# Performance work log

Measured on AMD Instinct MI355X. Metric: run time of the kernel, lower is better.

The kernel has to match this reference:

```python
import jax, jax.numpy as jnp
import numpy as np

D = 1024

def setup_inputs() -> dict:
    key = jax.random.key(0)
    ks = jax.random.split(key, 9)
    s = 1.0 / np.sqrt(D)
    x = jax.random.normal(ks[0], (8, 4096, D), dtype=jnp.float32)
    Wq = jax.random.uniform(ks[1], (D, D), jnp.float32, -s, s)
    bq = jax.random.uniform(ks[2], (D,), jnp.float32, -s, s)
    Wk = jax.random.uniform(ks[3], (D, D), jnp.float32, -s, s)
    bk = jax.random.uniform(ks[4], (D,), jnp.float32, -s, s)
    Wv = jax.random.uniform(ks[5], (D, D), jnp.float32, -s, s)
    bv = jax.random.uniform(ks[6], (D,), jnp.float32, -s, s)
    Wo = jax.random.uniform(ks[7], (D, D), jnp.float32, -s, s)
    bo = jax.random.uniform(ks[8], (D,), jnp.float32, -s, s)
    return {"x": x, "Wq": Wq, "bq": bq, "Wk": Wk, "bk": bk,
            "Wv": Wv, "bv": bv, "Wo": Wo, "bo": bo}

def reference(x, Wq, bq, Wk, bk, Wv, bv, Wo, bo):
    # Linear projections (torch Linear: x @ W.T + b)
    Q = x @ Wq.T + bq
    K = x @ Wk.T + bk
    V = x @ Wv.T + bv
    # elu+1 feature map (positive features)
    Q = jax.nn.elu(Q) + 1.0
    K = jax.nn.elu(K) + 1.0
    # KV outer-product accumulation over sequence: [b, d, e]
    KV = jnp.einsum('bnd,bne->bde', K, V)
    # normalizer Z: [b, n]
    Z = jnp.einsum('bnd,bd->bn', Q, K.sum(axis=1) + 1e-6)
    context = jnp.einsum('bnd,bde->bne', Q, KV) / Z[..., None]
    return context @ Wo.T + bo
```

## Files before the change

kernel.cpp:

```cpp
#include <hip/hip_runtime.h>
#include <stdint.h>

typedef unsigned short u16;
typedef __attribute__((ext_vector_type(8))) short short8;
typedef __attribute__((ext_vector_type(4))) float f32x4;

#define SEQ    4096
#define NB     8
#define DMODEL 1024
#define MTOT   (NB*SEQ)

static __device__ __forceinline__ float bf2f(u16 u){
  union { float f; uint32_t i; } v; v.i = ((uint32_t)u) << 16; return v.f;
}
static __device__ __forceinline__ u16 f2bf(float f){
  union { float f; uint32_t i; } v; v.f = f;
  uint32_t i = v.i + 0x7FFFu + ((v.i >> 16) & 1u);
  return (u16)(i >> 16);
}

static __device__ __forceinline__ void stage16(const void* g, void* l){
  __builtin_amdgcn_global_load_lds(
      (const __attribute__((address_space(1))) void*)g,
      (__attribute__((address_space(3))) void*)l,
      16, 0, 0);
}

__global__ void cvt_f32_bf16(const float* __restrict__ s, u16* __restrict__ d, int n){
  int i = (blockIdx.x * 256 + threadIdx.x) * 8;
  if (i >= n) return;
  float4 a = *(const float4*)(s + i);
  float4 b = *(const float4*)(s + i + 4);
  union { u16 h[8]; short8 v; } o;
  o.h[0]=f2bf(a.x); o.h[1]=f2bf(a.y); o.h[2]=f2bf(a.z); o.h[3]=f2bf(a.w);
  o.h[4]=f2bf(b.x); o.h[5]=f2bf(b.y); o.h[6]=f2bf(b.z); o.h[7]=f2bf(b.w);
  *(short8*)(d + i) = o.v;
}

__global__ __launch_bounds__(256)
void cvt_tr(const float* __restrict__ in, u16* __restrict__ outN,
            u16* __restrict__ outT, int R, int C)
{
  __shared__ float t[64][65];
  const int tid = threadIdx.x;
  const int ntc = C >> 6;
  const int tr = blockIdx.x / ntc, tc = blockIdx.x % ntc;
  const int r0 = tr << 6, c0 = tc << 6;
  const int lrow = tid >> 4, lc4 = (tid & 15) << 2;
  #pragma unroll
  for (int p = 0; p < 4; p++){
    float4 v = *(const float4*)(in + (size_t)(r0 + p*16 + lrow) * C + c0 + lc4);
    t[p*16 + lrow][lc4+0] = v.x; t[p*16 + lrow][lc4+1] = v.y;
    t[p*16 + lrow][lc4+2] = v.z; t[p*16 + lrow][lc4+3] = v.w;
  }
  __syncthreads();
  const int wrow = tid >> 3, wc8 = (tid & 7) << 3;
  if (outN){
    #pragma unroll
    for (int p = 0; p < 2; p++){
      int r = p*32 + wrow;
      union { u16 h[8]; short8 v; } o;
      #pragma unroll
      for (int j = 0; j < 8; j++) o.h[j] = f2bf(t[r][wc8 + j]);
      *(short8*)(outN + (size_t)(r0 + r) * C + c0 + wc8) = o.v;
    }
  }
  #pragma unroll
  for (int p = 0; p < 2; p++){
    int c = p*32 + wrow;
    union { u16 h[8]; short8 v; } o;
    #pragma unroll
    for (int j = 0; j < 8; j++) o.h[j] = f2bf(t[wc8 + j][c]);
    *(short8*)(outT + (size_t)(c0 + c) * R + r0 + wc8) = o.v;
  }
}

__global__ void bo2_kernel(const float* __restrict__ Wo, const float* __restrict__ bv,
                           const float* __restrict__ bo, float* __restrict__ bo2){
  int o = blockIdx.x * 4 + (threadIdx.x >> 6);
  int lane = threadIdx.x & 63;
  const float* row = Wo + (size_t)o * DMODEL;
  float s = 0.f;
  #pragma unroll
  for (int j = 0; j < 4; j++){
    float4 w = *(const float4*)(row + j*256 + lane*4);
    float4 b = *(const float4*)(bv  + j*256 + lane*4);
    s += w.x*b.x + w.y*b.y + w.z*b.z + w.w*b.w;
  }
  for (int off = 32; off; off >>= 1) s += __shfl_xor(s, off);
  if (lane == 0) bo2[o] = bo[o] + s;
}

__global__ void ksum_kernel(const u16* __restrict__ Kt, float* __restrict__ Ksum){
  int wid  = blockIdx.x * 4 + (threadIdx.x >> 6);
  int lane = threadIdx.x & 63;
  int d = wid & 1023, b = wid >> 10;
  const u16* row = Kt + (size_t)d * MTOT + (size_t)b * SEQ;
  float s = 0.f;
  #pragma unroll
  for (int j = 0; j < 8; j++){
    short8 v = *(const short8*)(row + j * 512 + lane * 8);
    #pragma unroll
    for (int t = 0; t < 8; t++) s += bf2f((u16)v[t]);
  }
  for (int off = 32; off; off >>= 1) s += __shfl_xor(s, off);
  if (lane == 0) Ksum[wid] = s + 1e-6f;
}

__global__ void z_kernel(const u16* __restrict__ Qb, const float* __restrict__ Ksum,
                         float* __restrict__ Z){
  int n    = blockIdx.x * 4 + (threadIdx.x >> 6);
  int lane = threadIdx.x & 63;
  const u16*   qrow = Qb + (size_t)n * DMODEL;
  const float* ks   = Ksum + (size_t)(n >> 12) * DMODEL;
  float s = 0.f;
  #pragma unroll
  for (int j = 0; j < 2; j++){
    int base = j * 512 + lane * 8;
    short8 q  = *(const short8*)(qrow + base);
    float4 k0 = *(const float4*)(ks + base);
    float4 k1 = *(const float4*)(ks + base + 4);
    s += bf2f((u16)q[0])*k0.x + bf2f((u16)q[1])*k0.y + bf2f((u16)q[2])*k0.z + bf2f((u16)q[3])*k0.w
       + bf2f((u16)q[4])*k1.x + bf2f((u16)q[5])*k1.y + bf2f((u16)q[6])*k1.z + bf2f((u16)q[7])*k1.w;
  }
  for (int off = 32; off; off >>= 1) s += __shfl_xor(s, off);
  if (lane == 0) Z[n] = s;
}

__global__ __launch_bounds__(256)
void gemm_bt(const u16* __restrict__ A, int ldA,
             const u16* __restrict__ BT, int ldBT, int Kdim,
             u16* __restrict__ Obf, int ldO)
{
  __shared__ u16 Al[128 * 32];
  __shared__ u16 Bl[128 * 32];
  const int tid  = threadIdx.x;
  const int lane = tid & 63;
  const int w    = tid >> 6;
  const int tcol = blockIdx.x;
  const int trow = blockIdx.y;

  const u16* Ap = A  + (size_t)trow * 128 * ldA;
  const u16* Bp = BT + (size_t)tcol * 128 * ldBT;

  f32x4 acc[4][4] = {};
  const int srow = (lane >> 2);
  const int scol = (lane & 3) * 8;

  for (int k0 = 0; k0 < Kdim; k0 += 32){
    #pragma unroll
    for (int i = 0; i < 2; i++){
      int r = w * 32 + i * 16 + srow;
      stage16(Ap + (size_t)r * ldA  + k0 + scol, (char*)Al + w * 2048 + i * 1024);
      stage16(Bp + (size_t)r * ldBT + k0 + scol, (char*)Bl + w * 2048 + i * 1024);
    }
    __syncthreads();
    const int mr = (w >> 1) * 64, nc = (w & 1) * 64;
    const int lr = lane & 15, lk = (lane >> 4) * 8;
    short8 av[4], bv[4];
    #pragma unroll
    for (int mi = 0; mi < 4; mi++) av[mi] = *(const short8*)&Al[(mr + mi*16 + lr)*32 + lk];
    #pragma unroll
    for (int nj = 0; nj < 4; nj++) bv[nj] = *(const short8*)&Bl[(nc + nj*16 + lr)*32 + lk];
    #pragma unroll
    for (int mi = 0; mi < 4; mi++)
      #pragma unroll
      for (int nj = 0; nj < 4; nj++)
        acc[mi][nj] = __builtin_amdgcn_mfma_f32_16x16x32_bf16(av[mi], bv[nj], acc[mi][nj], 0, 0, 0);
    __syncthreads();
  }

  const int mr = (w >> 1) * 64, nc = (w & 1) * 64;
  const int lr = lane & 15, lq = lane >> 4;
  #pragma unroll
  for (int mi = 0; mi < 4; mi++)
    #pragma unroll
    for (int r = 0; r < 4; r++){
      const size_t grow = (size_t)trow * 128 + mr + mi * 16 + lq * 4 + r;
      #pragma unroll
      for (int nj = 0; nj < 4; nj++){
        const size_t gcol = (size_t)tcol * 128 + nc + nj * 16 + lr;
        Obf[grow * ldO + gcol] = f2bf(acc[mi][nj][r]);
      }
    }
}

static __device__ __forceinline__ void stage_chunk(
    const u16* __restrict__ g, int ld, int k0, u16* smem, int baseU16, int tid){
  #pragma unroll
  for (int c = 0; c < 2; c++){
    int lin = c * 512 + tid;
    int row = lin >> 3;
    int slotL = (lin & 7) ^ (row & 7);
    stage16(g + (size_t)row * ld + k0 + slotL * 8,
            (char*)smem + baseU16 * 2 + (c * 8 + (tid >> 6)) * 1024);
  }
}

template<int EPI>
__global__ __launch_bounds__(512, 2)
void gemm8(const u16* __restrict__ A, int ldA,
           const u16* __restrict__ BT, int ldBT, int NT,
           const float* __restrict__ bias, const float* __restrict__ Zv,
           u16* __restrict__ Obf, float* __restrict__ Of32, int ldO)
{
  __shared__ u16 smem[65536];
  const int tid  = threadIdx.x;
  const int lane = tid & 63;
  const int w    = tid >> 6;
  const int wm   = w >> 2, wn = w & 3;
  const int lr   = lane & 15, kq = lane >> 4;

  const int nwg  = gridDim.x;
  const int orig = blockIdx.x;
  const int work = (orig & 7) * (nwg >> 3) + (orig >> 3);
  int trow, tcol; size_t boff = 0;
  if (EPI == 1)      { trow = work & 3; tcol = work >> 2; }
  else               { tcol = work & 3; trow = work >> 2;
                       if (EPI == 2) boff = (size_t)(trow >> 4) * 1024; }
  const int tileM = trow * 256, tileN = tcol * 256;

  const u16* Ag = A + (size_t)tileM * ldA;
  const u16* Bg = BT + boff + (size_t)tileN * ldBT;

  f32x4 acc[8][4] = {};

#define STAGE(buf, k0) do { \
    stage_chunk(Ag,                    ldA,  (k0), smem, (buf) + 0,     tid); \
    stage_chunk(Ag + (size_t)128*ldA,  ldA,  (k0), smem, (buf) + 8192,  tid); \
    stage_chunk(Bg,                    ldBT, (k0), smem, (buf) + 16384, tid); \
    stage_chunk(Bg + (size_t)128*ldBT, ldBT, (k0), smem, (buf) + 24576, tid); \
  } while(0)

#define LDSA(MF, KC) (*(const short8*)(smem + cb + (wm*128 + (MF)*16 + lr)*64 + ((((KC)*4 + kq) ^ (lr & 7)) * 8)))
#define LDSB(NF, KC) (*(const short8*)(smem + cb + 16384 + (wn*64 + (NF)*16 + lr)*64 + ((((KC)*4 + kq) ^ (lr & 7)) * 8)))

#define QUAD(M0, N0, AV, BV) do { \
  __builtin_amdgcn_s_setprio(1); \
  _Pragma("unroll") for (int mi = 0; mi < 4; mi++) \
    _Pragma("unroll") for (int ni = 0; ni < 2; ni++) \
      _Pragma("unroll") for (int kc = 0; kc < 2; kc++) \
        acc[(M0)+mi][(N0)+ni] = __builtin_amdgcn_mfma_f32_16x16x32_bf16( \
            AV[mi][kc], BV[ni][kc], acc[(M0)+mi][(N0)+ni], 0, 0, 0); \
  __builtin_amdgcn_s_setprio(0); \
} while(0)

  STAGE(0, 0);
  STAGE(32768, 64);
  asm volatile("s_waitcnt vmcnt(8)" ::: "memory");
  __builtin_amdgcn_s_barrier();

  for (int t = 0; t < NT; t++){
    const int cb  = (t & 1) << 15;
    const int kNN = (t + 2 < NT ? t + 2 : NT - 1) * 64;
    short8 a0[4][2], a1[4][2], bl[2][2], bh[2][2];

    #pragma unroll
    for (int i = 0; i < 4; i++){ a0[i][0] = LDSA(i, 0);   a0[i][1] = LDSA(i, 1); }
    #pragma unroll
    for (int i = 0; i < 2; i++){ bl[i][0] = LDSB(i, 0);   bl[i][1] = LDSB(i, 1); }
    __builtin_amdgcn_s_barrier();
    asm volatile("s_waitcnt lgkmcnt(0)" ::: "memory");
    QUAD(0, 0, a0, bl);
    __builtin_amdgcn_s_barrier();

    #pragma unroll
    for (int i = 0; i < 2; i++){ bh[i][0] = LDSB(2+i, 0); bh[i][1] = LDSB(2+i, 1); }
    __builtin_amdgcn_s_barrier();
    asm volatile("s_waitcnt lgkmcnt(0)" ::: "memory");
    QUAD(0, 2, a0, bh);
    __builtin_amdgcn_s_barrier();

    #pragma unroll
    for (int i = 0; i < 4; i++){ a1[i][0] = LDSA(4+i, 0); a1[i][1] = LDSA(4+i, 1); }
    stage_chunk(Bg, ldBT, kNN, smem, cb + 16384, tid);
    __builtin_amdgcn_s_barrier();
    asm volatile("s_waitcnt lgkmcnt(0)" ::: "memory");
    QUAD(4, 2, a1, bh);
    __builtin_amdgcn_s_barrier();

    stage_chunk(Bg + (size_t)128*ldBT, ldBT, kNN, smem, cb + 24576, tid);
    stage_chunk(Ag,                    ldA,  kNN, smem, cb + 0,     tid);
    stage_chunk(Ag + (size_t)128*ldA,  ldA,  kNN, smem, cb + 8192,  tid);
    QUAD(4, 0, a1, bl);
    asm volatile("s_waitcnt vmcnt(8)" ::: "memory");
    __builtin_amdgcn_s_barrier();
  }

#undef STAGE
#undef LDSA
#undef LDSB
#undef QUAD

  #pragma unroll
  for (int mf = 0; mf < 8; mf++){
    #pragma unroll
    for (int r = 0; r < 4; r++){
      const int grow = tileM + wm*128 + mf*16 + kq*4 + r;
      float rowB = 0.f, zin = 0.f;
      if (EPI == 1) rowB = bias[grow];
      if (EPI == 2) zin = 1.f / Zv[grow];
      #pragma unroll
      for (int nf = 0; nf < 4; nf++){
        const int gcol = tileN + wn*64 + nf*16 + lr;
        float v = acc[mf][nf][r];
        if (EPI == 0) { v += bias[gcol]; v = (v > 0.f) ? v + 1.f : __expf(v); }
        if (EPI == 1) { v += rowB;       v = (v > 0.f) ? v + 1.f : __expf(v); }
        if constexpr (EPI == 2) Of32[(size_t)grow * ldO + gcol] = v * zin + bias[gcol];
        else                    Obf [(size_t)grow * ldO + gcol] = f2bf(v);
      }
    }
  }
}

template<int EPI>
__global__ __launch_bounds__(512, 2)
void gemm8h(const u16* __restrict__ A, int ldA,
            const u16* __restrict__ BT, int ldBT, int NT,
            u16* __restrict__ Obf, int ldO)
{
  __shared__ u16 smem[49152];
  const int tid  = threadIdx.x;
  const int lane = tid & 63;
  const int w    = tid >> 6;
  const int wm   = w >> 2, wn = w & 3;
  const int lr   = lane & 15, kq = lane >> 4;

  const int orig = blockIdx.x;
  const int work = (orig & 7) * 32 + (orig >> 3);
  int trow, tcol; size_t aoff = 0, boff = 0, ooff = 0;
  if (EPI == 3) { int zb = work >> 5, sub = work & 31;
                  trow = sub & 7; tcol = sub >> 3;
                  aoff = (size_t)zb * SEQ; boff = aoff; ooff = (size_t)zb << 20; }
  else          { trow = work & 7; tcol = work >> 3; }
  const int tileM = trow * 128, tileN = tcol * 256;

  const u16* Ag = A  + aoff + (size_t)tileM * ldA;
  const u16* Bg = BT + boff + (size_t)tileN * ldBT;

  f32x4 acc[4][4] = {};

#define STAGEH(buf, k0) do { \
    stage_chunk(Ag,                    ldA,  (k0), smem, (buf) + 0,     tid); \
    stage_chunk(Bg,                    ldBT, (k0), smem, (buf) + 8192,  tid); \
    stage_chunk(Bg + (size_t)128*ldBT, ldBT, (k0), smem, (buf) + 16384, tid); \
  } while(0)

#define LDSAH(MF, KC) (*(const short8*)(smem + cb + (wm*64 + (MF)*16 + lr)*64 + ((((KC)*4 + kq) ^ (lr & 7)) * 8)))
#define LDSBH(NF, KC) (*(const short8*)(smem + cb + 8192 + (wn*64 + (NF)*16 + lr)*64 + ((((KC)*4 + kq) ^ (lr & 7)) * 8)))

  STAGEH(0, 0);
  STAGEH(24576, 64);
  asm volatile("s_waitcnt vmcnt(6)" ::: "memory");
  __builtin_amdgcn_sched_barrier(0);
  __builtin_amdgcn_s_barrier();

  for (int t = 0; t < NT; t++){
    const int cb = (t & 1) * 24576;
    short8 af[4][2], bf[4][2];
    #pragma unroll
    for (int i = 0; i < 4; i++){ af[i][0] = LDSAH(i, 0); af[i][1] = LDSAH(i, 1); }
    #pragma unroll
    for (int i = 0; i < 4; i++){ bf[i][0] = LDSBH(i, 0); bf[i][1] = LDSBH(i, 1); }
    __builtin_amdgcn_s_setprio(1);
    #pragma unroll
    for (int mi = 0; mi < 4; mi++)
      #pragma unroll
      for (int nj = 0; nj < 4; nj++)
        #pragma unroll
        for (int kc = 0; kc < 2; kc++)
          acc[mi][nj] = __builtin_amdgcn_mfma_f32_16x16x32_bf16(
              af[mi][kc], bf[nj][kc], acc[mi][nj], 0, 0, 0);
    __builtin_amdgcn_s_setprio(0);
    __builtin_amdgcn_sched_barrier(0);
    __builtin_amdgcn_s_barrier();
    const int kNN = (t + 2 < NT ? t + 2 : NT - 1) * 64;
    STAGEH(cb, kNN);
    asm volatile("s_waitcnt vmcnt(6)" ::: "memory");
    __builtin_amdgcn_sched_barrier(0);
    __builtin_amdgcn_s_barrier();
  }
#undef STAGEH
#undef LDSAH
#undef LDSBH

  #pragma unroll
  for (int mf = 0; mf < 4; mf++){
    #pragma unroll
    for (int r = 0; r < 4; r++){
      const int grow = tileM + wm*64 + mf*16 + kq*4 + r;
      #pragma unroll
      for (int nf = 0; nf < 4; nf++){
        const int gcol = tileN + wn*64 + nf*16 + lr;
        Obf[ooff + (size_t)grow * ldO + gcol] = f2bf(acc[mf][nf][r]);
      }
    }
  }
}

extern "C" void kernel_launch(void* const* d_in, const int* in_sizes, int n_in,
                              void* d_out, int out_size, void* d_ws, size_t ws_size,
                              hipStream_t stream)
{
  const float* x  = (const float*)d_in[0];
  const float* Wq = (const float*)d_in[1];
  const float* bq = (const float*)d_in[2];
  const float* Wk = (const float*)d_in[3];
  const float* bk = (const float*)d_in[4];
  const float* Wv = (const float*)d_in[5];
  const float* bv = (const float*)d_in[6];
  const float* Wo = (const float*)d_in[7];
  const float* bo = (const float*)d_in[8];
  float* out = (float*)d_out;

  char* ws = (char*)d_ws;
  u16*   xb  = (u16*)(ws + 0);
  u16*   Tt  = (u16*)(ws + 0);
  u16*   Gt  = (u16*)(ws + 16777216);
  u16*   xT  = (u16*)(ws + 67108864);
  u16*   Qb  = (u16*)(ws + 134217728);
  u16*   Kt  = (u16*)(ws + 201326592);
  u16*   Wqb = (u16*)(ws + 268435456);
  u16*   Wkb = (u16*)(ws + 270532608);
  u16*   Wob = (u16*)(ws + 272629760);
  u16*   WvT = (u16*)(ws + 274726912);
  u16*   W2b = (u16*)(ws + 276824064);
  float* Ks  = (float*)(ws + 278921216);
  float* Zp  = (float*)(ws + 278953984);
  float* bo2 = (float*)(ws + 279085056);

  cvt_tr<<<8192, 256, 0, stream>>>(x, xb, xT, MTOT, DMODEL);
  cvt_f32_bf16<<<512, 256, 0, stream>>>(Wq, Wqb, DMODEL * DMODEL);
  cvt_f32_bf16<<<512, 256, 0, stream>>>(Wk, Wkb, DMODEL * DMODEL);
  cvt_f32_bf16<<<512, 256, 0, stream>>>(Wo, Wob, DMODEL * DMODEL);
  cvt_tr<<<256, 256, 0, stream>>>(Wv, (u16*)nullptr, WvT, DMODEL, DMODEL);
  bo2_kernel<<<256, 256, 0, stream>>>(Wo, bv, bo, bo2);
  gemm_bt<<<dim3(8, 8, 1), dim3(256), 0, stream>>>(Wob, 1024, WvT, 1024, 1024,
                                                   W2b, 1024);

  gemm8<0><<<512, 512, 0, stream>>>(xb, 1024, Wqb, 1024, 16, bq, nullptr,
                                    Qb, nullptr, 1024);
  gemm8<1><<<512, 512, 0, stream>>>(Wkb, 1024, xb, 1024, 16, bk, nullptr,
                                    Kt, nullptr, MTOT);
  ksum_kernel<<<2048, 256, 0, stream>>>(Kt, Ks);
  z_kernel<<<8192, 256, 0, stream>>>(Qb, Ks, Zp);
  gemm8h<3><<<256, 512, 0, stream>>>(Kt, MTOT, xT, MTOT, 64, Tt, 1024);
  gemm8h<4><<<256, 512, 0, stream>>>(W2b, 1024, Tt, 1024, 16, Gt, 8192);
  gemm8<2><<<512, 512, 0, stream>>>(Qb, 1024, Gt, 8192, 16, bo2, Zp,
                                    nullptr, out, 1024);
}
```

Measured before the change: 428.7 us.

## Fuse K-sum and Z normalizer reductions into projection GEMM epilogues

Removes the separate ksum and z kernels. The K-sum and Z dot products are now computed inside the K- and Q-projection GEMM epilogues using shuffle reductions and atomicAdd, after a memset of the accumulators. Each gemm8 block now computes two adjacent 256-column tiles in sequence, keeping the A rows in the pipeline, and the grid is halved to 256 blocks. The cost is atomic contention and order-dependent float sums, and the K GEMM must now run before the Q GEMM. Halving the grid may also leave CUs underused.

```diff
diff --git a/kernel.cpp b/kernel.cpp
--- a/kernel.cpp
+++ b/kernel.cpp
@@ -89,42 +89,6 @@
   }
   for (int off = 32; off; off >>= 1) s += __shfl_xor(s, off);
   if (lane == 0) bo2[o] = bo[o] + s;
-}
-
-__global__ void ksum_kernel(const u16* __restrict__ Kt, float* __restrict__ Ksum){
-  int wid  = blockIdx.x * 4 + (threadIdx.x >> 6);
-  int lane = threadIdx.x & 63;
-  int d = wid & 1023, b = wid >> 10;
-  const u16* row = Kt + (size_t)d * MTOT + (size_t)b * SEQ;
-  float s = 0.f;
-  #pragma unroll
-  for (int j = 0; j < 8; j++){
-    short8 v = *(const short8*)(row + j * 512 + lane * 8);
-    #pragma unroll
-    for (int t = 0; t < 8; t++) s += bf2f((u16)v[t]);
-  }
-  for (int off = 32; off; off >>= 1) s += __shfl_xor(s, off);
-  if (lane == 0) Ksum[wid] = s + 1e-6f;
-}
-
-__global__ void z_kernel(const u16* __restrict__ Qb, const float* __restrict__ Ksum,
-                         float* __restrict__ Z){
-  int n    = blockIdx.x * 4 + (threadIdx.x >> 6);
-  int lane = threadIdx.x & 63;
-  const u16*   qrow = Qb + (size_t)n * DMODEL;
-  const float* ks   = Ksum + (size_t)(n >> 12) * DMODEL;
-  float s = 0.f;
-  #pragma unroll
-  for (int j = 0; j < 2; j++){
-    int base = j * 512 + lane * 8;
-    short8 q  = *(const short8*)(qrow + base);
-    float4 k0 = *(const float4*)(ks + base);
-    float4 k1 = *(const float4*)(ks + base + 4);
-    s += bf2f((u16)q[0])*k0.x + bf2f((u16)q[1])*k0.y + bf2f((u16)q[2])*k0.z + bf2f((u16)q[3])*k0.w
-       + bf2f((u16)q[4])*k1.x + bf2f((u16)q[5])*k1.y + bf2f((u16)q[6])*k1.z + bf2f((u16)q[7])*k1.w;
-  }
-  for (int off = 32; off; off >>= 1) s += __shfl_xor(s, off);
-  if (lane == 0) Z[n] = s;
 }
 
 __global__ __launch_bounds__(256)
@@ -200,9 +164,10 @@
 template<int EPI>
 __global__ __launch_bounds__(512, 2)
 void gemm8(const u16* __restrict__ A, int ldA,
-           const u16* __restrict__ BT, int ldBT, int NT,
+           const u16* __restrict__ BT, int ldBT,
            const float* __restrict__ bias, const float* __restrict__ Zv,
-           u16* __restrict__ Obf, float* __restrict__ Of32, int ldO)
+           u16* __restrict__ Obf, float* __restrict__ Of32, int ldO,
+           float* __restrict__ redOut)
 {
   __shared__ u16 smem[65536];
   const int tid  = threadIdx.x;
@@ -211,26 +176,18 @@
   const int wm   = w >> 2, wn = w & 3;
   const int lr   = lane & 15, kq = lane >> 4;
 
-  const int nwg  = gridDim.x;
   const int orig = blockIdx.x;
-  const int work = (orig & 7) * (nwg >> 3) + (orig >> 3);
-  int trow, tcol; size_t boff = 0;
-  if (EPI == 1)      { trow = work & 3; tcol = work >> 2; }
-  else               { tcol = work & 3; trow = work >> 2;
-                       if (EPI == 2) boff = (size_t)(trow >> 4) * 1024; }
-  const int tileM = trow * 256, tileN = tcol * 256;
-
-  const u16* Ag = A + (size_t)tileM * ldA;
-  const u16* Bg = BT + boff + (size_t)tileN * ldBT;
+  const int work = (orig & 7) * 32 + (orig >> 3);
+  int trow, tcp; size_t boff = 0;
+  if (EPI == 1) { trow = work & 3; tcp = work >> 2; }
+  else          { tcp = work & 1; trow = work >> 1;
+                  if (EPI == 2) boff = (size_t)(trow >> 4) * 1024; }
+  const int tileM = trow * 256;
+
+  const u16* Ag  = A + (size_t)tileM * ldA;
+  const u16* Bg0 = BT + boff + (size_t)(tcp * 512) * ldBT;
 
   f32x4 acc[8][4] = {};
-
-#define STAGE(buf, k0) do { \
-    stage_chunk(Ag,                    ldA,  (k0), smem, (buf) + 0,     tid); \
-    stage_chunk(Ag + (size_t)128*ldA,  ldA,  (k0), smem, (buf) + 8192,  tid); \
-    stage_chunk(Bg,                    ldBT, (k0), smem, (buf) + 16384, tid); \
-    stage_chunk(Bg + (size_t)128*ldBT, ldBT, (k0), smem, (buf) + 24576, tid); \
-  } while(0)
 
 #define LDSA(MF, KC) (*(const short8*)(smem + cb + (wm*128 + (MF)*16 + lr)*64 + ((((KC)*4 + kq) ^ (lr & 7)) * 8)))
 #define LDSB(NF, KC) (*(const short8*)(smem + cb + 16384 + (wn*64 + (NF)*16 + lr)*64 + ((((KC)*4 + kq) ^ (lr & 7)) * 8)))
@@ -245,14 +202,51 @@
   __builtin_amdgcn_s_setprio(0); \
 } while(0)
 
-  STAGE(0, 0);
-  STAGE(32768, 64);
+#define EPILOG(TILEN) do { \
+  _Pragma("unroll") for (int mf = 0; mf < 8; mf++){ \
+    _Pragma("unroll") for (int r = 0; r < 4; r++){ \
+      const int grow = tileM + wm*128 + mf*16 + kq*4 + r; \
+      float rowB = 0.f, zin = 0.f, red = 0.f; \
+      if (EPI == 1) rowB = bias[grow]; \
+      if (EPI == 2) zin = 1.f / Zv[grow]; \
+      _Pragma("unroll") for (int nf = 0; nf < 4; nf++){ \
+        const int gcol = (TILEN) + wn*64 + nf*16 + lr; \
+        float v = acc[mf][nf][r]; \
+        if (EPI == 0){ v += bias[gcol]; v = (v > 0.f) ? v + 1.f : __expf(v); \
+                       red += v * (Zv[(grow >> 12)*1024 + gcol] + 1e-6f); } \
+        if (EPI == 1){ v += rowB; v = (v > 0.f) ? v + 1.f : __expf(v); red += v; } \
+        if (EPI == 2) Of32[(size_t)grow * ldO + gcol] = v * zin + bias[gcol]; \
+        else          Obf [(size_t)grow * ldO + gcol] = f2bf(v); \
+      } \
+      if (EPI == 0 || EPI == 1){ \
+        red += __shfl_xor(red, 1); red += __shfl_xor(red, 2); \
+        red += __shfl_xor(red, 4); red += __shfl_xor(red, 8); \
+        if (lr == 0){ \
+          if (EPI == 0) atomicAdd(&redOut[grow], red); \
+          else          atomicAdd(&redOut[((TILEN) >> 12)*1024 + grow], red); \
+        } \
+      } \
+    } \
+  } \
+} while(0)
+
+  stage_chunk(Ag,                     ldA,  0,  smem, 0,     tid);
+  stage_chunk(Ag + (size_t)128*ldA,   ldA,  0,  smem, 8192,  tid);
+  stage_chunk(Bg0,                    ldBT, 0,  smem, 16384, tid);
+  stage_chunk(Bg0 + (size_t)128*ldBT, ldBT, 0,  smem, 24576, tid);
+  stage_chunk(Ag,                     ldA,  64, smem, 32768 + 0,     tid);
+  stage_chunk(Ag + (size_t)128*ldA,   ldA,  64, smem, 32768 + 8192,  tid);
+  stage_chunk(Bg0,                    ldBT, 64, smem, 32768 + 16384, tid);
+  stage_chunk(Bg0 + (size_t)128*ldBT, ldBT, 64, smem, 32768 + 24576, tid);
   asm volatile("s_waitcnt vmcnt(8)" ::: "memory");
   __builtin_amdgcn_s_barrier();
 
-  for (int t = 0; t < NT; t++){
-    const int cb  = (t & 1) << 15;
-    const int kNN = (t + 2 < NT ? t + 2 : NT - 1) * 64;
+  for (int t = 0; t < 32; t++){
+    const int cb = (t & 1) << 15;
+    int s = t + 2; if (s > 31) s = 31;
+    const int ks = (s & 15) * 64;
+    const u16* As = Ag;
+    const u16* Bs = Bg0 + (size_t)((s >> 4) * 256) * ldBT;
     short8 a0[4][2], a1[4][2], bl[2][2], bh[2][2];
 
     #pragma unroll
@@ -273,44 +267,35 @@
 
     #pragma unroll
     for (int i = 0; i < 4; i++){ a1[i][0] = LDSA(4+i, 0); a1[i][1] = LDSA(4+i, 1); }
-    stage_chunk(Bg, ldBT, kNN, smem, cb + 16384, tid);
+    stage_chunk(Bs, ldBT, ks, smem, cb + 16384, tid);
     __builtin_amdgcn_s_barrier();
     asm volatile("s_waitcnt lgkmcnt(0)" ::: "memory");
     QUAD(4, 2, a1, bh);
     __builtin_amdgcn_s_barrier();
 
-    stage_chunk(Bg + (size_t)128*ldBT, ldBT, kNN, smem, cb + 24576, tid);
-    stage_chunk(Ag,                    ldA,  kNN, smem, cb + 0,     tid);
-    stage_chunk(Ag + (size_t)128*ldA,  ldA,  kNN, smem, cb + 8192,  tid);
+    stage_chunk(Bs + (size_t)128*ldBT, ldBT, ks, smem, cb + 24576, tid);
+    stage_chunk(As,                    ldA,  ks, smem, cb + 0,     tid);
+    stage_chunk(As + (size_t)128*ldA,  ldA,  ks, smem, cb + 8192,  tid);
     QUAD(4, 0, a1, bl);
     asm volatile("s_waitcnt vmcnt(8)" ::: "memory");
     __builtin_amdgcn_s_barrier();
-  }
-
-#undef STAGE
+
+    if (t == 15){
+      EPILOG(tcp * 512);
+      #pragma unroll
+      for (int mf = 0; mf < 8; mf++)
+        #pragma unroll
+        for (int nf = 0; nf < 4; nf++)
+          acc[mf][nf] = (f32x4){0.f, 0.f, 0.f, 0.f};
+    }
+  }
+
+  EPILOG(tcp * 512 + 256);
+
 #undef LDSA
 #undef LDSB
 #undef QUAD
-
-  #pragma unroll
-  for (int mf = 0; mf < 8; mf++){
-    #pragma unroll
-    for (int r = 0; r < 4; r++){
-      const int grow = tileM + wm*128 + mf*16 + kq*4 + r;
-      float rowB = 0.f, zin = 0.f;
-      if (EPI == 1) rowB = bias[grow];
-      if (EPI == 2) zin = 1.f / Zv[grow];
-      #pragma unroll
-      for (int nf = 0; nf < 4; nf++){
-        const int gcol = tileN + wn*64 + nf*16 + lr;
-        float v = acc[mf][nf][r];
-        if (EPI == 0) { v += bias[gcol]; v = (v > 0.f) ? v + 1.f : __expf(v); }
-        if (EPI == 1) { v += rowB;       v = (v > 0.f) ? v + 1.f : __expf(v); }
-        if constexpr (EPI == 2) Of32[(size_t)grow * ldO + gcol] = v * zin + bias[gcol];
-        else                    Obf [(size_t)grow * ldO + gcol] = f2bf(v);
-      }
-    }
-  }
+#undef EPILOG
 }
 
 template<int EPI>
@@ -437,15 +422,15 @@
   bo2_kernel<<<256, 256, 0, stream>>>(Wo, bv, bo, bo2);
   gemm_bt<<<dim3(8, 8, 1), dim3(256), 0, stream>>>(Wob, 1024, WvT, 1024, 1024,
                                                    W2b, 1024);
-
-  gemm8<0><<<512, 512, 0, stream>>>(xb, 1024, Wqb, 1024, 16, bq, nullptr,
-                                    Qb, nullptr, 1024);
-  gemm8<1><<<512, 512, 0, stream>>>(Wkb, 1024, xb, 1024, 16, bk, nullptr,
-                                    Kt, nullptr, MTOT);
-  ksum_kernel<<<2048, 256, 0, stream>>>(Kt, Ks);
-  z_kernel<<<8192, 256, 0, stream>>>(Qb, Ks, Zp);
+  hipMemsetAsync(Ks, 0, NB * DMODEL * sizeof(float), stream);
+  hipMemsetAsync(Zp, 0, MTOT * sizeof(float), stream);
+
+  gemm8<1><<<256, 512, 0, stream>>>(Wkb, 1024, xb, 1024, bk, nullptr,
+                                    Kt, nullptr, MTOT, Ks);
+  gemm8<0><<<256, 512, 0, stream>>>(xb, 1024, Wqb, 1024, bq, Ks,
+                                    Qb, nullptr, 1024, Zp);
   gemm8h<3><<<256, 512, 0, stream>>>(Kt, MTOT, xT, MTOT, 64, Tt, 1024);
   gemm8h<4><<<256, 512, 0, stream>>>(W2b, 1024, Tt, 1024, 16, Gt, 8192);
-  gemm8<2><<<512, 512, 0, stream>>>(Qb, 1024, Gt, 8192, 16, bo2, Zp,
-                                    nullptr, out, 1024);
-}
+  gemm8<2><<<256, 512, 0, stream>>>(Qb, 1024, Gt, 8192, bo2, Zp,
+                                    nullptr, out, 1024, nullptr);
+}
```

New measurement: 582.2 us. +35.8%, slower.

## Fuse K column-sum and Z normalizer into GEMM epilogues via atomics

Applied to the files above, without the earlier changes.

Removes the separate ksum and z kernels. The K-projection GEMM epilogue now accumulates per-batch column sums of K with shuffle reductions and atomicAdd, and the Q-projection GEMM, reordered to run after K, computes Z from those sums in its epilogue. This saves re-reading the Kt and Qb buffers and two launches. In exchange it adds two memsets, atomic contention, nondeterministic float summation order, and a small epsilon-placement difference (1e-6 added per element inside the dot product).

```diff
diff --git a/kernel.cpp b/kernel.cpp
--- a/kernel.cpp
+++ b/kernel.cpp
@@ -89,42 +89,6 @@
   }
   for (int off = 32; off; off >>= 1) s += __shfl_xor(s, off);
   if (lane == 0) bo2[o] = bo[o] + s;
-}
-
-__global__ void ksum_kernel(const u16* __restrict__ Kt, float* __restrict__ Ksum){
-  int wid  = blockIdx.x * 4 + (threadIdx.x >> 6);
-  int lane = threadIdx.x & 63;
-  int d = wid & 1023, b = wid >> 10;
-  const u16* row = Kt + (size_t)d * MTOT + (size_t)b * SEQ;
-  float s = 0.f;
-  #pragma unroll
-  for (int j = 0; j < 8; j++){
-    short8 v = *(const short8*)(row + j * 512 + lane * 8);
-    #pragma unroll
-    for (int t = 0; t < 8; t++) s += bf2f((u16)v[t]);
-  }
-  for (int off = 32; off; off >>= 1) s += __shfl_xor(s, off);
-  if (lane == 0) Ksum[wid] = s + 1e-6f;
-}
-
-__global__ void z_kernel(const u16* __restrict__ Qb, const float* __restrict__ Ksum,
-                         float* __restrict__ Z){
-  int n    = blockIdx.x * 4 + (threadIdx.x >> 6);
-  int lane = threadIdx.x & 63;
-  const u16*   qrow = Qb + (size_t)n * DMODEL;
-  const float* ks   = Ksum + (size_t)(n >> 12) * DMODEL;
-  float s = 0.f;
-  #pragma unroll
-  for (int j = 0; j < 2; j++){
-    int base = j * 512 + lane * 8;
-    short8 q  = *(const short8*)(qrow + base);
-    float4 k0 = *(const float4*)(ks + base);
-    float4 k1 = *(const float4*)(ks + base + 4);
-    s += bf2f((u16)q[0])*k0.x + bf2f((u16)q[1])*k0.y + bf2f((u16)q[2])*k0.z + bf2f((u16)q[3])*k0.w
-       + bf2f((u16)q[4])*k1.x + bf2f((u16)q[5])*k1.y + bf2f((u16)q[6])*k1.z + bf2f((u16)q[7])*k1.w;
-  }
-  for (int off = 32; off; off >>= 1) s += __shfl_xor(s, off);
-  if (lane == 0) Z[n] = s;
 }
 
 __global__ __launch_bounds__(256)
@@ -202,7 +166,8 @@
 void gemm8(const u16* __restrict__ A, int ldA,
            const u16* __restrict__ BT, int ldBT, int NT,
            const float* __restrict__ bias, const float* __restrict__ Zv,
-           u16* __restrict__ Obf, float* __restrict__ Of32, int ldO)
+           u16* __restrict__ Obf, float* __restrict__ Of32, int ldO,
+           float* __restrict__ redOut)
 {
   __shared__ u16 smem[65536];
   const int tid  = threadIdx.x;
@@ -297,17 +262,27 @@
     #pragma unroll
     for (int r = 0; r < 4; r++){
       const int grow = tileM + wm*128 + mf*16 + kq*4 + r;
-      float rowB = 0.f, zin = 0.f;
+      float rowB = 0.f, zin = 0.f, red = 0.f;
       if (EPI == 1) rowB = bias[grow];
       if (EPI == 2) zin = 1.f / Zv[grow];
       #pragma unroll
       for (int nf = 0; nf < 4; nf++){
         const int gcol = tileN + wn*64 + nf*16 + lr;
         float v = acc[mf][nf][r];
-        if (EPI == 0) { v += bias[gcol]; v = (v > 0.f) ? v + 1.f : __expf(v); }
-        if (EPI == 1) { v += rowB;       v = (v > 0.f) ? v + 1.f : __expf(v); }
+        if (EPI == 0){ v += bias[gcol]; v = (v > 0.f) ? v + 1.f : __expf(v);
+                       red += v * (Zv[(grow >> 12)*1024 + gcol] + 1e-6f); }
+        if (EPI == 1){ v += rowB;       v = (v > 0.f) ? v + 1.f : __expf(v);
+                       red += v; }
         if constexpr (EPI == 2) Of32[(size_t)grow * ldO + gcol] = v * zin + bias[gcol];
         else                    Obf [(size_t)grow * ldO + gcol] = f2bf(v);
+      }
+      if (EPI == 0 || EPI == 1){
+        red += __shfl_xor(red, 1); red += __shfl_xor(red, 2);
+        red += __shfl_xor(red, 4); red += __shfl_xor(red, 8);
+        if (lr == 0){
+          if (EPI == 0) atomicAdd(&redOut[grow], red);
+          else          atomicAdd(&redOut[(tileN >> 12)*1024 + grow], red);
+        }
       }
     }
   }
@@ -437,15 +412,15 @@
   bo2_kernel<<<256, 256, 0, stream>>>(Wo, bv, bo, bo2);
   gemm_bt<<<dim3(8, 8, 1), dim3(256), 0, stream>>>(Wob, 1024, WvT, 1024, 1024,
                                                    W2b, 1024);
-
-  gemm8<0><<<512, 512, 0, stream>>>(xb, 1024, Wqb, 1024, 16, bq, nullptr,
-                                    Qb, nullptr, 1024);
+  hipMemsetAsync(Ks, 0, NB * DMODEL * sizeof(float), stream);
+  hipMemsetAsync(Zp, 0, MTOT * sizeof(float), stream);
+
   gemm8<1><<<512, 512, 0, stream>>>(Wkb, 1024, xb, 1024, 16, bk, nullptr,
-                                    Kt, nullptr, MTOT);
-  ksum_kernel<<<2048, 256, 0, stream>>>(Kt, Ks);
-  z_kernel<<<8192, 256, 0, stream>>>(Qb, Ks, Zp);
+                                    Kt, nullptr, MTOT, Ks);
+  gemm8<0><<<512, 512, 0, stream>>>(xb, 1024, Wqb, 1024, 16, bq, Ks,
+                                    Qb, nullptr, 1024, Zp);
   gemm8h<3><<<256, 512, 0, stream>>>(Kt, MTOT, xT, MTOT, 64, Tt, 1024);
   gemm8h<4><<<256, 512, 0, stream>>>(W2b, 1024, Tt, 1024, 16, Gt, 8192);
   gemm8<2><<<512, 512, 0, stream>>>(Qb, 1024, Gt, 8192, 16, bo2, Zp,
-                                    nullptr, out, 1024);
-}
+                                    nullptr, out, 1024, nullptr);
+}
```

Measured after the change: 436.5 us. No clear change (+1.8%).
